# Performance work log

Hardware: AMD Instinct MI355X
Metric: run time of the kernel (lower is better)

## Reference

```python
import jax, jax.numpy as jnp
import numpy as np

D_MODEL = 1024
D_KV = 64
N_HEADS = 16
INNER = N_HEADS * D_KV
EPS = 1e-6


def setup_inputs() -> dict:
    key = jax.random.key(0)
    ks = jax.random.split(key, 8)
    B, SQ, SKV = 2, 2048, 4096
    hidden_states = jax.random.normal(ks[0], (B, SQ, D_MODEL), dtype=jnp.float32)
    key_value_states = jax.random.normal(ks[1], (B, SKV, D_MODEL), dtype=jnp.float32)
    attention_mask = jnp.zeros((B, 1, 1, SKV), dtype=jnp.float32)
    # nn.Linear(in, out, bias=False): y = x @ W.T; store W as [in, out] here
    s = 0.02
    Wq = jax.random.normal(ks[2], (D_MODEL, INNER), dtype=jnp.float32) * s
    Wk = jax.random.normal(ks[3], (D_MODEL, INNER), dtype=jnp.float32) * s
    Wv = jax.random.normal(ks[4], (D_MODEL, INNER), dtype=jnp.float32) * s
    Wo = jax.random.normal(ks[5], (INNER, D_MODEL), dtype=jnp.float32) * s
    ln_weight = jnp.ones((D_MODEL,), dtype=jnp.float32)
    return {
        "hidden_states": hidden_states,
        "key_value_states": key_value_states,
        "attention_mask": attention_mask,
        "ln_weight": ln_weight,
        "Wq": Wq,
        "Wk": Wk,
        "Wv": Wv,
        "Wo": Wo,
    }


def _t5_rmsnorm(x, w, eps=EPS):
    # no mean subtraction, variance in fp32
    var = jnp.mean(jnp.square(x.astype(jnp.float32)), axis=-1, keepdims=True)
    return w * (x * jax.lax.rsqrt(var + eps)).astype(x.dtype)


def reference(hidden_states, key_value_states, attention_mask, ln_weight, Wq, Wk, Wv, Wo):
    B, SQ, _ = hidden_states.shape
    SKV = key_value_states.shape[1]
    normed = _t5_rmsnorm(hidden_states, ln_weight)

    # projections -> [B, H, S, Dk]
    q = (normed @ Wq).reshape(B, SQ, N_HEADS, D_KV).transpose(0, 2, 1, 3)
    k = (key_value_states @ Wk).reshape(B, SKV, N_HEADS, D_KV).transpose(0, 2, 1, 3)
    v = (key_value_states @ Wv).reshape(B, SKV, N_HEADS, D_KV).transpose(0, 2, 1, 3)

    # T5: NO 1/sqrt(d) scaling
    scores = jnp.einsum("bhqd,bhkd->bhqk", q, k) + attention_mask
    attn = jax.nn.softmax(scores.astype(jnp.float32), axis=-1).astype(scores.dtype)
    ctx = jnp.einsum("bhqk,bhkd->bhqd", attn, v)
    ctx = ctx.transpose(0, 2, 1, 3).reshape(B, SQ, INNER)
    attn_out = ctx @ Wo
    return hidden_states + attn_out
```

## Files before the change

kernel.cpp:

```cpp
#include <hip/hip_runtime.h>

typedef unsigned short u16;
typedef unsigned int u32;
typedef __attribute__((ext_vector_type(4))) float f32x4;
typedef __attribute__((ext_vector_type(8))) short short8;
typedef __attribute__((ext_vector_type(4))) short short4v;

#define BB   2
#define SQL  2048
#define SKVL 4096
#define DM   1024
#define NH   16
#define DK   64
#define L2E  1.44269504f

#if __has_builtin(__builtin_amdgcn_exp2f)
#define EXP2(x) __builtin_amdgcn_exp2f(x)
#else
#define EXP2(x) exp2f(x)
#endif

#define MFMA32(a, b, c) __builtin_amdgcn_mfma_f32_16x16x32_bf16(a, b, c, 0, 0, 0)
#define MFMA16(a, b, c) __builtin_amdgcn_mfma_f32_16x16x16bf16_1k(a, b, c, 0, 0, 0)

__device__ __forceinline__ u16 f2bf(float f) {
  union { float f; unsigned u; } v; v.f = f;
  unsigned r = v.u + 0x7fff + ((v.u >> 16) & 1);
  return (u16)(r >> 16);
}

__device__ __forceinline__ short4v pack4(float p0, float p1, float p2, float p3) {
  union { float f; u32 u; } a, b, c, d;
  a.f = p0; b.f = p1; c.f = p2; d.f = p3;
  union { uint2 v; short4v s; } r;
  r.v.x = __builtin_amdgcn_perm(b.u + 0x8000u, a.u + 0x8000u, 0x07060302);
  r.v.y = __builtin_amdgcn_perm(d.u + 0x8000u, c.u + 0x8000u, 0x07060302);
  return r.s;
}

__device__ __forceinline__ void gload16(const void* g, void* lds) {
  __builtin_amdgcn_global_load_lds(
      (const __attribute__((address_space(1))) unsigned int*)g,
      (__attribute__((address_space(3))) unsigned int*)lds, 16, 0, 0);
}

__global__ void pre_kernel(const float* __restrict__ hidden, const float* __restrict__ lnw,
                           const float* __restrict__ kvs,
                           const float* __restrict__ Wq, const float* __restrict__ Wk,
                           const float* __restrict__ Wv, const float* __restrict__ Wo,
                           u16* __restrict__ normed, u16* __restrict__ kvb,
                           u16* __restrict__ Wqt, u16* __restrict__ Wkt,
                           u16* __restrict__ Wvt, u16* __restrict__ Wot) {
  __shared__ float red[4];
  __shared__ float tile[32][33];
  int bid = blockIdx.x, t = threadIdx.x;
  if (bid < 4096) {
    int row = bid;
    float4 v = ((const float4*)(hidden + (size_t)row * DM))[t];
    float ss = v.x * v.x + v.y * v.y + v.z * v.z + v.w * v.w;
#pragma unroll
    for (int m = 32; m >= 1; m >>= 1) ss += __shfl_xor(ss, m, 64);
    int lane = t & 63, wv = t >> 6;
    if (lane == 0) red[wv] = ss;
    __syncthreads();
    float total = red[0] + red[1] + red[2] + red[3];
    float scale = rsqrtf(total * (1.0f / DM) + 1e-6f);
    float4 g = ((const float4*)lnw)[t];
    ushort4 o;
    o.x = f2bf(v.x * scale * g.x);
    o.y = f2bf(v.y * scale * g.y);
    o.z = f2bf(v.z * scale * g.z);
    o.w = f2bf(v.w * scale * g.w);
    ((ushort4*)(normed + (size_t)row * DM))[t] = o;
  } else if (bid < 12288) {
    int i = (bid - 4096) * 256 + t;
    float4 v = ((const float4*)kvs)[i];
    ushort4 o;
    o.x = f2bf(v.x); o.y = f2bf(v.y); o.z = f2bf(v.z); o.w = f2bf(v.w);
    ((ushort4*)kvb)[i] = o;
  } else {
    int g = bid - 12288;
    int z = g >> 10;
    const float* W = (z == 0) ? Wq : (z == 1) ? Wk : (z == 2) ? Wv : Wo;
    u16* Wt = (z == 0) ? Wqt : (z == 1) ? Wkt : (z == 2) ? Wvt : Wot;
    int xx = g & 31, yy = (g >> 5) & 31;
    int tx = t & 31, ty = t >> 5;
    int k0 = yy * 32, n0 = xx * 32;
#pragma unroll
    for (int i = 0; i < 4; i++)
      tile[ty + i * 8][tx] = W[(size_t)(k0 + ty + i * 8) * DM + n0 + tx];
    __syncthreads();
#pragma unroll
    for (int i = 0; i < 4; i++)
      Wt[(size_t)(n0 + ty + i * 8) * DM + k0 + tx] = f2bf(tile[tx][ty + i * 8]);
  }
}

__global__ __launch_bounds__(256, 2) void proj_kernel(
    const u16* __restrict__ normed, const u16* __restrict__ kvb,
    const u16* __restrict__ Wqt, const u16* __restrict__ Wkt,
    const u16* __restrict__ Wvt,
    u16* __restrict__ Qb, u16* __restrict__ Kbf, u16* __restrict__ Vtb) {
  const int K = 1024;
  __shared__ __align__(16) u16 Al[2 * 8192];
  __shared__ __align__(16) u16 Bl[2 * 8192];
  int tid = threadIdx.x, lane = tid & 63, w = tid >> 6;
  int l15 = lane & 15, quad = lane >> 4;
  int wy = w >> 1, wx = w & 1;

  int bid = blockIdx.x;
  int mode;
  const u16 *A, *Bt;
  int tm, tn;
  if (bid < 256) {
    mode = 0; A = normed; Bt = Wqt;
    int xcd = bid & 7, j = bid >> 3;
    tm = ((j >> 3) * 8 + xcd) * 128; tn = (j & 7) * 128;
  } else if (bid < 768) {
    mode = 1; A = kvb; Bt = Wkt;
    int kid = bid - 256;
    int xcd = kid & 7, j = kid >> 3;
    tm = ((j >> 3) * 8 + xcd) * 128; tn = (j & 7) * 128;
  } else {
    mode = 2; A = Wvt; Bt = kvb;
    int vid = bid - 768;
    int xcd = vid & 7, j = vid >> 3;
    tn = ((j >> 3) * 8 + xcd) * 128; tm = (j & 7) * 128;
  }

  auto stage = [&](int k0, int buf) {
    u16* Ad = Al + buf * 8192;
    u16* Bd = Bl + buf * 8192;
#pragma unroll
    for (int r = 0; r < 2; r++) {
      int mg = w * 2 + r;
      const u16* ar = A + (size_t)(tm + mg * 16 + l15) * K + k0 + quad * 8;
      const u16* br = Bt + (size_t)(tn + mg * 16 + l15) * K + k0 + quad * 8;
      gload16(ar, &Ad[mg * 512]);
      gload16(ar + 32, &Ad[4096 + mg * 512]);
      gload16(br, &Bd[mg * 512]);
      gload16(br + 32, &Bd[4096 + mg * 512]);
    }
  };

  f32x4 acc[4][4] = {};
  stage(0, 0);
  for (int it = 0; it < 16; ++it) {
    __syncthreads();
    if (it + 1 < 16) stage((it + 1) * 64, (it + 1) & 1);
    const u16* Ag = Al + (it & 1) * 8192;
    const u16* Bg = Bl + (it & 1) * 8192;
#pragma unroll
    for (int c = 0; c < 2; c++) {
      short8 af[4], bfr[4];
#pragma unroll
      for (int i = 0; i < 4; i++) {
        af[i] = *(const short8*)&Ag[c * 4096 + ((wy * 4 + i) * 64 + lane) * 8];
        bfr[i] = *(const short8*)&Bg[c * 4096 + ((wx * 4 + i) * 64 + lane) * 8];
      }
#pragma unroll
      for (int mt = 0; mt < 4; mt++)
#pragma unroll
        for (int nt = 0; nt < 4; nt++)
          acc[mt][nt] = MFMA32(af[mt], bfr[nt], acc[mt][nt]);
    }
  }

#pragma unroll
  for (int mt = 0; mt < 4; mt++) {
    int m0 = tm + wy * 64 + mt * 16 + quad * 4;
#pragma unroll
    for (int nt = 0; nt < 4; nt++) {
      int n = tn + wx * 64 + nt * 16 + l15;
      if (mode == 0) {
#pragma unroll
        for (int r = 0; r < 4; r++)
          Qb[(size_t)(m0 + r) * 1024 + n] = f2bf(acc[mt][nt][r] * L2E);
      } else if (mode == 1) {
#pragma unroll
        for (int r = 0; r < 4; r++)
          Kbf[(size_t)(m0 + r) * 1024 + n] = f2bf(acc[mt][nt][r]);
      } else {
        int b = n >> 12, skv = n & 4095;
        int kvt = skv >> 6, kvl = skv & 63;
        int p = kvl >> 5, kth = (kvl >> 4) & 1, qd = (kvl >> 2) & 3, elo = kvl & 3;
        int e = kth * 4 + elo;
        int h = m0 >> 6, d0 = m0 & 63;
        size_t base = ((size_t)((b * NH + h) * 64 + kvt) << 12) + (size_t)(p * 4 + qd) * 512 + e;
#pragma unroll
        for (int r = 0; r < 4; r++)
          Vtb[base + (size_t)(d0 + r) * 8] = f2bf(acc[mt][nt][r]);
      }
    }
  }
}

__global__ __launch_bounds__(256, 2) void flash_kernel(
    const u16* __restrict__ Qp, const u16* __restrict__ Kp, const u16* __restrict__ Vtb,
    const float* __restrict__ mask, u16* __restrict__ ctx) {
  __shared__ __align__(16) char smem[65536];
  u16* Kbuf = (u16*)smem;
  u16* Vbuf = (u16*)(smem + 32768);
  float* Ox = (float*)smem;
  float* Ll = (float*)(smem + 32768);

  int tid = threadIdx.x, lane = tid & 63, w = tid >> 6;
  int l15 = lane & 15, quad = lane >> 4;
  int grp = w >> 1, wg = w & 1;
  int qb = blockIdx.x, bh = blockIdx.y;
  int b = bh >> 4, h = bh & 15;
  int q0 = qb * 128 + wg * 64;

  short8 qf[4][2];
#pragma unroll
  for (int mt = 0; mt < 4; mt++)
#pragma unroll
    for (int kf = 0; kf < 2; kf++)
      qf[mt][kf] = *(const short8*)(Qp + (size_t)(b * SQL + q0 + mt * 16 + l15) * DM +
                                    h * DK + kf * 32 + quad * 8);

  f32x4 of[4][4] = {};
  f32x4 la[4] = {};
  const short4v ones = {0x3F80, 0x3F80, 0x3F80, 0x3F80};

  const size_t vblob = (size_t)(b * NH + h) * 64 * 4096;
  const float* mrow = mask + (size_t)b * SKVL;

  auto stage = [&](int tileIdx, int buf) {
    int kv0 = tileIdx * 64;
    u16* Kd = Kbuf + (buf * 2 + grp) * 4096;
    u16* Vd = Vbuf + (buf * 2 + grp) * 4096;
#pragma unroll
    for (int r = 0; r < 4; r++) {
      int u = wg * 4 + r;
      int kt = u >> 1, kf = u & 1;
      gload16(Kp + (size_t)(b * SKVL + kv0 + kt * 16 + l15) * DM + h * DK + kf * 32 + quad * 8,
              &Kd[u * 512]);
      gload16(Vtb + vblob + (size_t)tileIdx * 4096 + u * 512 + lane * 8, &Vd[u * 512]);
    }
  };

  f32x4 mlc[4], mln[4];
  {
    int kv0 = grp * 64;
#pragma unroll
    for (int kt = 0; kt < 4; kt++)
      mlc[kt] = *(const f32x4*)(mrow + kv0 + kt * 16 + quad * 4) * L2E;
  }
  stage(grp, 0);

  for (int it = 0; it < 32; ++it) {
    __syncthreads();
    if (it + 1 < 32) {
      stage((it + 1) * 2 + grp, (it + 1) & 1);
      int kvn = ((it + 1) * 2 + grp) * 64;
#pragma unroll
      for (int kt = 0; kt < 4; kt++)
        mln[kt] = *(const f32x4*)(mrow + kvn + kt * 16 + quad * 4) * L2E;
    }
    const u16* Kg = Kbuf + ((it & 1) * 2 + grp) * 4096;
    const u16* Vg = Vbuf + ((it & 1) * 2 + grp) * 4096;

#pragma unroll
    for (int ktp = 0; ktp < 2; ktp++) {
      short4v pa[2][4];
#pragma unroll
      for (int kth = 0; kth < 2; kth++) {
        int kt = ktp * 2 + kth;
        short8 k0 = *(const short8*)&Kg[((kt * 2 + 0) * 64 + lane) * 8];
        short8 k1 = *(const short8*)&Kg[((kt * 2 + 1) * 64 + lane) * 8];
#pragma unroll
        for (int mt = 0; mt < 4; mt++) {
          f32x4 st = mlc[kt];
          st = MFMA32(k0, qf[mt][0], st);
          st = MFMA32(k1, qf[mt][1], st);
          pa[kth][mt] = pack4(EXP2(st[0]), EXP2(st[1]), EXP2(st[2]), EXP2(st[3]));
        }
      }
#pragma unroll
      for (int mt = 0; mt < 4; mt++) {
        la[mt] = MFMA16(pa[0][mt], ones, la[mt]);
        la[mt] = MFMA16(pa[1][mt], ones, la[mt]);
      }
#pragma unroll
      for (int nt = 0; nt < 4; nt++) {
        short8 vv = *(const short8*)&Vg[((ktp * 4 + quad) * 64 + nt * 16 + l15) * 8];
        short4v vlo = {vv[0], vv[1], vv[2], vv[3]};
        short4v vhi = {vv[4], vv[5], vv[6], vv[7]};
#pragma unroll
        for (int mt = 0; mt < 4; mt++) {
          of[mt][nt] = MFMA16(pa[0][mt], vlo, of[mt][nt]);
          of[mt][nt] = MFMA16(pa[1][mt], vhi, of[mt][nt]);
        }
      }
    }
#pragma unroll
    for (int kt = 0; kt < 4; kt++) mlc[kt] = mln[kt];
  }

  __syncthreads();
  if (grp == 1) {
#pragma unroll
    for (int mt = 0; mt < 4; mt++) {
#pragma unroll
      for (int nt = 0; nt < 4; nt++)
#pragma unroll
        for (int r = 0; r < 4; r++)
          Ox[(wg * 64 + mt * 16 + quad * 4 + r) * 64 + nt * 16 + l15] = of[mt][nt][r];
      if (l15 == 0)
#pragma unroll
        for (int r = 0; r < 4; r++) Ll[wg * 64 + mt * 16 + quad * 4 + r] = la[mt][r];
    }
  }
  __syncthreads();
  if (grp == 0) {
#pragma unroll
    for (int mt = 0; mt < 4; mt++)
#pragma unroll
      for (int r = 0; r < 4; r++) {
        int ql = wg * 64 + mt * 16 + quad * 4 + r;
        float inv = 1.0f / (la[mt][r] + Ll[ql]);
        int q = qb * 128 + ql;
#pragma unroll
        for (int nt = 0; nt < 4; nt++) {
          float ov = of[mt][nt][r] + Ox[ql * 64 + nt * 16 + l15];
          ctx[(size_t)(b * SQL + q) * DM + h * DK + nt * 16 + l15] = f2bf(ov * inv);
        }
      }
  }
}

__global__ __launch_bounds__(256, 2) void ogemm_kernel(
    const u16* __restrict__ A, const u16* __restrict__ Bt,
    float* __restrict__ C, const float* __restrict__ resid) {
  const int K = 1024;
  __shared__ __align__(16) u16 Al[2 * 8192];
  __shared__ __align__(16) u16 Bl[2 * 8192];
  int tid = threadIdx.x, lane = tid & 63, w = tid >> 6;
  int l15 = lane & 15, quad = lane >> 4;
  int wy = w >> 1, wx = w & 1;
  int bid = blockIdx.x;
  int xcd = bid & 7, j = bid >> 3;
  int tm = ((j >> 3) * 8 + xcd) * 128, tn = (j & 7) * 128;

  auto stage = [&](int k0, int buf) {
    u16* Ad = Al + buf * 8192;
    u16* Bd = Bl + buf * 8192;
#pragma unroll
    for (int r = 0; r < 2; r++) {
      int mg = w * 2 + r;
      const u16* ar = A + (size_t)(tm + mg * 16 + l15) * K + k0 + quad * 8;
      const u16* br = Bt + (size_t)(tn + mg * 16 + l15) * K + k0 + quad * 8;
      gload16(ar, &Ad[mg * 512]);
      gload16(ar + 32, &Ad[4096 + mg * 512]);
      gload16(br, &Bd[mg * 512]);
      gload16(br + 32, &Bd[4096 + mg * 512]);
    }
  };

  f32x4 acc[4][4] = {};
  stage(0, 0);
  for (int it = 0; it < 16; ++it) {
    __syncthreads();
    if (it + 1 < 16) stage((it + 1) * 64, (it + 1) & 1);
    const u16* Ag = Al + (it & 1) * 8192;
    const u16* Bg = Bl + (it & 1) * 8192;
#pragma unroll
    for (int c = 0; c < 2; c++) {
      short8 af[4], bfr[4];
#pragma unroll
      for (int i = 0; i < 4; i++) {
        af[i] = *(const short8*)&Ag[c * 4096 + ((wy * 4 + i) * 64 + lane) * 8];
        bfr[i] = *(const short8*)&Bg[c * 4096 + ((wx * 4 + i) * 64 + lane) * 8];
      }
#pragma unroll
      for (int mt = 0; mt < 4; mt++)
#pragma unroll
        for (int nt = 0; nt < 4; nt++)
          acc[mt][nt] = MFMA32(af[mt], bfr[nt], acc[mt][nt]);
    }
  }

#pragma unroll
  for (int mt = 0; mt < 4; mt++) {
    int m0 = tm + wy * 64 + mt * 16 + quad * 4;
#pragma unroll
    for (int nt = 0; nt < 4; nt++) {
      int n = tn + wx * 64 + nt * 16 + l15;
#pragma unroll
      for (int r = 0; r < 4; r++) {
        size_t idx = (size_t)(m0 + r) * 1024 + n;
        C[idx] = resid[idx] + acc[mt][nt][r];
      }
    }
  }
}

extern "C" void kernel_launch(void* const* d_in, const int* in_sizes, int n_in,
                              void* d_out, int out_size, void* d_ws, size_t ws_size,
                              hipStream_t stream) {
  const float* hidden = (const float*)d_in[0];
  const float* kvs    = (const float*)d_in[1];
  const float* mask   = (const float*)d_in[2];
  const float* lnw    = (const float*)d_in[3];
  const float* Wq     = (const float*)d_in[4];
  const float* Wk     = (const float*)d_in[5];
  const float* Wv     = (const float*)d_in[6];
  const float* Wo     = (const float*)d_in[7];
  char* ws = (char*)d_ws;

  u16* normed = (u16*)(ws + 0);
  u16* kvb    = (u16*)(ws + 8388608);
  u16* Wqt    = (u16*)(ws + 25165824);
  u16* Wkt    = (u16*)(ws + 27262976);
  u16* Wvt    = (u16*)(ws + 29360128);
  u16* Wot    = (u16*)(ws + 31457280);
  u16* Qb     = (u16*)(ws + 33554432);
  u16* Kbf    = (u16*)(ws + 41943040);
  u16* Vtb    = (u16*)(ws + 58720256);
  u16* ctxb   = (u16*)(ws + 75497472);

  pre_kernel<<<16384, 256, 0, stream>>>(hidden, lnw, kvs, Wq, Wk, Wv, Wo,
                                        normed, kvb, Wqt, Wkt, Wvt, Wot);
  proj_kernel<<<1280, 256, 0, stream>>>(normed, kvb, Wqt, Wkt, Wvt, Qb, Kbf, Vtb);
  flash_kernel<<<dim3(SQL / 128, BB * NH), 256, 0, stream>>>(Qb, Kbf, Vtb, mask, ctxb);
  ogemm_kernel<<<256, 256, 0, stream>>>(ctxb, Wot, (float*)d_out, hidden);
}
```

Measured before the change: 347.7 us.

## Use 256x128 GEMM tiles with K-step 32 in projection and output kernels

Changes the projection and output GEMMs from 128x128 tiles with K-step 64 to 256x128 tiles with K-step 32. Each wave now owns 64 rows across the full 128 columns, so every B fragment read from LDS is reused by all four waves and accumulators grow to 4x8. This raises arithmetic intensity per block and removes the XCD-aware tile swizzle. The cost is halving the grid (640 and 128 blocks), which may underfill the 256 CUs for the output GEMM, plus twice as many barrier iterations and higher register pressure.

```diff
diff --git a/kernel.cpp b/kernel.cpp
--- a/kernel.cpp
+++ b/kernel.cpp
@@ -103,75 +103,69 @@
     u16* __restrict__ Qb, u16* __restrict__ Kbf, u16* __restrict__ Vtb) {
   const int K = 1024;
   __shared__ __align__(16) u16 Al[2 * 8192];
-  __shared__ __align__(16) u16 Bl[2 * 8192];
+  __shared__ __align__(16) u16 Bl[2 * 4096];
   int tid = threadIdx.x, lane = tid & 63, w = tid >> 6;
   int l15 = lane & 15, quad = lane >> 4;
-  int wy = w >> 1, wx = w & 1;
 
   int bid = blockIdx.x;
   int mode;
   const u16 *A, *Bt;
   int tm, tn;
-  if (bid < 256) {
+  if (bid < 128) {
     mode = 0; A = normed; Bt = Wqt;
-    int xcd = bid & 7, j = bid >> 3;
-    tm = ((j >> 3) * 8 + xcd) * 128; tn = (j & 7) * 128;
-  } else if (bid < 768) {
+    tm = (bid & 15) * 256; tn = (bid >> 4) * 128;
+  } else if (bid < 384) {
     mode = 1; A = kvb; Bt = Wkt;
-    int kid = bid - 256;
-    int xcd = kid & 7, j = kid >> 3;
-    tm = ((j >> 3) * 8 + xcd) * 128; tn = (j & 7) * 128;
+    int kid = bid - 128;
+    tm = (kid & 31) * 256; tn = (kid >> 5) * 128;
   } else {
     mode = 2; A = Wvt; Bt = kvb;
-    int vid = bid - 768;
-    int xcd = vid & 7, j = vid >> 3;
-    tn = ((j >> 3) * 8 + xcd) * 128; tm = (j & 7) * 128;
+    int vid = bid - 384;
+    tn = (vid & 63) * 128; tm = (vid >> 6) * 256;
   }
 
   auto stage = [&](int k0, int buf) {
     u16* Ad = Al + buf * 8192;
-    u16* Bd = Bl + buf * 8192;
+    u16* Bd = Bl + buf * 4096;
+#pragma unroll
+    for (int r = 0; r < 4; r++) {
+      int u = w * 4 + r;
+      gload16(A + (size_t)(tm + u * 16 + l15) * K + k0 + quad * 8, &Ad[u * 512]);
+    }
 #pragma unroll
     for (int r = 0; r < 2; r++) {
-      int mg = w * 2 + r;
-      const u16* ar = A + (size_t)(tm + mg * 16 + l15) * K + k0 + quad * 8;
-      const u16* br = Bt + (size_t)(tn + mg * 16 + l15) * K + k0 + quad * 8;
-      gload16(ar, &Ad[mg * 512]);
-      gload16(ar + 32, &Ad[4096 + mg * 512]);
-      gload16(br, &Bd[mg * 512]);
-      gload16(br + 32, &Bd[4096 + mg * 512]);
+      int u = w * 2 + r;
+      gload16(Bt + (size_t)(tn + u * 16 + l15) * K + k0 + quad * 8, &Bd[u * 512]);
     }
   };
 
-  f32x4 acc[4][4] = {};
+  f32x4 acc[4][8] = {};
   stage(0, 0);
-  for (int it = 0; it < 16; ++it) {
+  for (int it = 0; it < 32; ++it) {
     __syncthreads();
-    if (it + 1 < 16) stage((it + 1) * 64, (it + 1) & 1);
+    if (it + 1 < 32) stage((it + 1) * 32, (it + 1) & 1);
     const u16* Ag = Al + (it & 1) * 8192;
-    const u16* Bg = Bl + (it & 1) * 8192;
-#pragma unroll
-    for (int c = 0; c < 2; c++) {
-      short8 af[4], bfr[4];
-#pragma unroll
-      for (int i = 0; i < 4; i++) {
-        af[i] = *(const short8*)&Ag[c * 4096 + ((wy * 4 + i) * 64 + lane) * 8];
-        bfr[i] = *(const short8*)&Bg[c * 4096 + ((wx * 4 + i) * 64 + lane) * 8];
-      }
-#pragma unroll
-      for (int mt = 0; mt < 4; mt++)
-#pragma unroll
-        for (int nt = 0; nt < 4; nt++)
-          acc[mt][nt] = MFMA32(af[mt], bfr[nt], acc[mt][nt]);
-    }
+    const u16* Bg = Bl + (it & 1) * 4096;
+    short8 af[4], bfr[8];
+#pragma unroll
+    for (int i = 0; i < 4; i++)
+      af[i] = *(const short8*)&Ag[((w * 4 + i) * 64 + lane) * 8];
+#pragma unroll
+    for (int j = 0; j < 8; j++)
+      bfr[j] = *(const short8*)&Bg[(j * 64 + lane) * 8];
+#pragma unroll
+    for (int mt = 0; mt < 4; mt++)
+#pragma unroll
+      for (int nt = 0; nt < 8; nt++)
+        acc[mt][nt] = MFMA32(af[mt], bfr[nt], acc[mt][nt]);
   }
 
 #pragma unroll
   for (int mt = 0; mt < 4; mt++) {
-    int m0 = tm + wy * 64 + mt * 16 + quad * 4;
-#pragma unroll
-    for (int nt = 0; nt < 4; nt++) {
-      int n = tn + wx * 64 + nt * 16 + l15;
+    int m0 = tm + w * 64 + mt * 16 + quad * 4;
+#pragma unroll
+    for (int nt = 0; nt < 8; nt++) {
+      int n = tn + nt * 16 + l15;
       if (mode == 0) {
 #pragma unroll
         for (int r = 0; r < 4; r++)
@@ -335,58 +329,54 @@
     float* __restrict__ C, const float* __restrict__ resid) {
   const int K = 1024;
   __shared__ __align__(16) u16 Al[2 * 8192];
-  __shared__ __align__(16) u16 Bl[2 * 8192];
+  __shared__ __align__(16) u16 Bl[2 * 4096];
   int tid = threadIdx.x, lane = tid & 63, w = tid >> 6;
   int l15 = lane & 15, quad = lane >> 4;
-  int wy = w >> 1, wx = w & 1;
   int bid = blockIdx.x;
-  int xcd = bid & 7, j = bid >> 3;
-  int tm = ((j >> 3) * 8 + xcd) * 128, tn = (j & 7) * 128;
+  int tm = (bid & 15) * 256, tn = (bid >> 4) * 128;
 
   auto stage = [&](int k0, int buf) {
     u16* Ad = Al + buf * 8192;
-    u16* Bd = Bl + buf * 8192;
+    u16* Bd = Bl + buf * 4096;
+#pragma unroll
+    for (int r = 0; r < 4; r++) {
+      int u = w * 4 + r;
+      gload16(A + (size_t)(tm + u * 16 + l15) * K + k0 + quad * 8, &Ad[u * 512]);
+    }
 #pragma unroll
     for (int r = 0; r < 2; r++) {
-      int mg = w * 2 + r;
-      const u16* ar = A + (size_t)(tm + mg * 16 + l15) * K + k0 + quad * 8;
-      const u16* br = Bt + (size_t)(tn + mg * 16 + l15) * K + k0 + quad * 8;
-      gload16(ar, &Ad[mg * 512]);
-      gload16(ar + 32, &Ad[4096 + mg * 512]);
-      gload16(br, &Bd[mg * 512]);
-      gload16(br + 32, &Bd[4096 + mg * 512]);
+      int u = w * 2 + r;
+      gload16(Bt + (size_t)(tn + u * 16 + l15) * K + k0 + quad * 8, &Bd[u * 512]);
     }
   };
 
-  f32x4 acc[4][4] = {};
+  f32x4 acc[4][8] = {};
   stage(0, 0);
-  for (int it = 0; it < 16; ++it) {
+  for (int it = 0; it < 32; ++it) {
     __syncthreads();
-    if (it + 1 < 16) stage((it + 1) * 64, (it + 1) & 1);
+    if (it + 1 < 32) stage((it + 1) * 32, (it + 1) & 1);
     const u16* Ag = Al + (it & 1) * 8192;
-    const u16* Bg = Bl + (it & 1) * 8192;
-#pragma unroll
-    for (int c = 0; c < 2; c++) {
-      short8 af[4], bfr[4];
-#pragma unroll
-      for (int i = 0; i < 4; i++) {
-        af[i] = *(const short8*)&Ag[c * 4096 + ((wy * 4 + i) * 64 + lane) * 8];
-        bfr[i] = *(const short8*)&Bg[c * 4096 + ((wx * 4 + i) * 64 + lane) * 8];
-      }
-#pragma unroll
-      for (int mt = 0; mt < 4; mt++)
-#pragma unroll
-        for (int nt = 0; nt < 4; nt++)
-          acc[mt][nt] = MFMA32(af[mt], bfr[nt], acc[mt][nt]);
-    }
+    const u16* Bg = Bl + (it & 1) * 4096;
+    short8 af[4], bfr[8];
+#pragma unroll
+    for (int i = 0; i < 4; i++)
+      af[i] = *(const short8*)&Ag[((w * 4 + i) * 64 + lane) * 8];
+#pragma unroll
+    for (int j = 0; j < 8; j++)
+      bfr[j] = *(const short8*)&Bg[(j * 64 + lane) * 8];
+#pragma unroll
+    for (int mt = 0; mt < 4; mt++)
+#pragma unroll
+      for (int nt = 0; nt < 8; nt++)
+        acc[mt][nt] = MFMA32(af[mt], bfr[nt], acc[mt][nt]);
   }
 
 #pragma unroll
   for (int mt = 0; mt < 4; mt++) {
-    int m0 = tm + wy * 64 + mt * 16 + quad * 4;
-#pragma unroll
-    for (int nt = 0; nt < 4; nt++) {
-      int n = tn + wx * 64 + nt * 16 + l15;
+    int m0 = tm + w * 64 + mt * 16 + quad * 4;
+#pragma unroll
+    for (int nt = 0; nt < 8; nt++) {
+      int n = tn + nt * 16 + l15;
 #pragma unroll
       for (int r = 0; r < 4; r++) {
         size_t idx = (size_t)(m0 + r) * 1024 + n;
@@ -422,7 +412,7 @@
 
   pre_kernel<<<16384, 256, 0, stream>>>(hidden, lnw, kvs, Wq, Wk, Wv, Wo,
                                         normed, kvb, Wqt, Wkt, Wvt, Wot);
-  proj_kernel<<<1280, 256, 0, stream>>>(normed, kvb, Wqt, Wkt, Wvt, Qb, Kbf, Vtb);
+  proj_kernel<<<640, 256, 0, stream>>>(normed, kvb, Wqt, Wkt, Wvt, Qb, Kbf, Vtb);
   flash_kernel<<<dim3(SQL / 128, BB * NH), 256, 0, stream>>>(Qb, Kbf, Vtb, mask, ctxb);
-  ogemm_kernel<<<256, 256, 0, stream>>>(ctxb, Wot, (float*)d_out, hidden);
-}
+  ogemm_kernel<<<128, 256, 0, stream>>>(ctxb, Wot, (float*)d_out, hidden);
+}
```

After: 361.7 us. 1.04x slower.
